# Optimization experiments

Hardware: AMD Instinct MI355X
Metric: run time of the kernel (lower is better)

Reference implementation:

```python
import jax, jax.numpy as jnp
import numpy as np
from jax import lax

B, H, V, L = 128, 256, 130, 100  # batch, hidden_size, vocab per stream, decode length


def _gru(x, h, wih, whh, bih, bhh):
    # torch.nn.GRUCell math
    gi = x @ wih.T + bih
    gh = h @ whh.T + bhh
    ir, iz, inn = jnp.split(gi, 3, axis=-1)
    hr, hz, hn = jnp.split(gh, 3, axis=-1)
    r = jax.nn.sigmoid(ir + hr)
    u = jax.nn.sigmoid(iz + hz)
    n = jnp.tanh(inn + r * hn)
    return (1.0 - u) * n + u * h


def _forward(z, gru1_wih, gru1_whh, gru1_bih, gru1_bhh,
             gru2_wih, gru2_whh, gru2_bih, gru2_bhh,
             ctx_wih, ctx_whh, ctx_bih, ctx_bhh,
             out_w, out_b, hid_w, hid_b, emb, length):
    b = z.shape[0]
    hidden = jnp.tanh(z @ hid_w.T + hid_b)                      # [B,H]
    h3 = jnp.broadcast_to(hidden[None], (3, b, hidden.shape[-1]))
    note0 = jnp.broadcast_to(emb[:, 0][:, None, :], (3, b, emb.shape[-1]))  # embed index 0
    vgru = jax.vmap(_gru)  # over the 3 parallel streams

    def step(carry, _):
        g1h, g2h, context, note = carry
        zb = jnp.broadcast_to(z[None], note.shape)
        g1h = vgru(jnp.concatenate([note, zb], -1), g1h,
                   gru1_wih, gru1_whh, gru1_bih, gru1_bhh)       # [3,B,H]
        unroll = g1h
        logits = []
        for i in range(3):  # fixed structural unroll (3 streams)
            ctx_in = jnp.concatenate([unroll[0], unroll[1], unroll[2]], -1)  # [B,3H]
            context = _gru(ctx_in, context, ctx_wih, ctx_whh, ctx_bih, ctx_bhh)
            h2 = _gru(jnp.concatenate([context, z], -1), g2h[i],
                      gru2_wih[i], gru2_whh[i], gru2_bih[i], gru2_bhh[i])
            g2h = g2h.at[i].set(h2)
            lg = (unroll[i] + h2) @ out_w[i].T + out_b[i]        # [B,V]
            logits.append(lg)
            ni = emb[i][jnp.argmax(lg, axis=-1)]                 # greedy sample -> embed
            note = note.at[i].set(ni)
            # NOTE: original code uses self.gru1[1] here (fixed index 1) -- kept faithful
            unroll = unroll.at[i].set(_gru(jnp.concatenate([ni, z], -1), unroll[i],
                                           gru1_wih[1], gru1_whh[1], gru1_bih[1], gru1_bhh[1]))
        return (g1h, g2h, context, note), jnp.stack(logits)     # [3,B,V]

    _, ys = lax.scan(step, (h3, h3, hidden, note0), None, length=length)
    return jnp.transpose(ys, (1, 2, 0, 3))                      # [3,B,L,V]


def setup_inputs() -> dict:
    key = jax.random.key(0)
    ks = jax.random.split(key, 18)
    s = 0.05
    n = lambda k, shp: jax.random.normal(k, shp, jnp.float32) * s
    return {
        "z": jax.random.normal(ks[0], (B, H), jnp.float32),
        "gru1_wih": n(ks[1], (3, 3 * H, 2 * H)),
        "gru1_whh": n(ks[2], (3, 3 * H, H)),
        "gru1_bih": n(ks[3], (3, 3 * H)),
        "gru1_bhh": n(ks[4], (3, 3 * H)),
        "gru2_wih": n(ks[5], (3, 3 * H, 2 * H)),
        "gru2_whh": n(ks[6], (3, 3 * H, H)),
        "gru2_bih": n(ks[7], (3, 3 * H)),
        "gru2_bhh": n(ks[8], (3, 3 * H)),
        "ctx_wih": n(ks[9], (3 * H, 3 * H)),
        "ctx_whh": n(ks[10], (3 * H, H)),
        "ctx_bih": n(ks[11], (3 * H,)),
        "ctx_bhh": n(ks[12], (3 * H,)),
        "out_w": n(ks[13], (3, V, H)),
        "out_b": n(ks[14], (3, V)),
        "hid_w": n(ks[15], (H, H)),
        "hid_b": n(ks[16], (H,)),
        "emb": n(ks[17], (3, V, H)),
        "length": L,
    }


def reference(z, gru1_wih, gru1_whh, gru1_bih, gru1_bhh,
              gru2_wih, gru2_whh, gru2_bih, gru2_bhh,
              ctx_wih, ctx_whh, ctx_bih, ctx_bhh,
              out_w, out_b, hid_w, hid_b, emb, length):
    return _forward(z, gru1_wih, gru1_whh, gru1_bih, gru1_bhh,
                    gru2_wih, gru2_whh, gru2_bih, gru2_bhh,
                    ctx_wih, ctx_whh, ctx_bih, ctx_bhh,
                    out_w, out_b, hid_w, hid_b, emb, length)
```

## Files before the change

### kernel.cpp

```cpp
#include <hip/hip_runtime.h>
#include <math.h>

#define B 128
#define H 256
#define V 130
#define L 100
#define G3 768

__device__ __forceinline__ float sigmoidf_(float x) { return 1.0f / (1.0f + expf(-x)); }

template <int NCHUNK>
__global__ __launch_bounds__(256) void gru_gates(
    const float* __restrict__ x0, const float* __restrict__ x1,
    const float* __restrict__ x2, const float* __restrict__ x3,
    const float* __restrict__ wih, int wih_k,
    const float* __restrict__ whh,
    const float* __restrict__ zadd, const float* __restrict__ bih,
    const float* __restrict__ bhh,
    float* __restrict__ out0, float* __restrict__ out1)
{
  __shared__ float xs[32][260];
  const int tid = threadIdx.x;
  const int r   = tid & 31;
  const int hc  = tid >> 5;
  const int row0 = blockIdx.y * 32;
  const int col  = blockIdx.x * 8 + hc;

  float giR = 0.f, giZ = 0.f, giN = 0.f;
  float ghR = 0.f, ghZ = 0.f, ghN = 0.f;
  float hold = 0.f;

  for (int c = 0; c < NCHUNK; ++c) {
    const float* src = (c == 0) ? x0 : (c == 1) ? x1 : (c == 2) ? x2 : x3;
    for (int j = tid; j < 32 * 64; j += 256) {
      const int rr = j >> 6, k4 = (j & 63) << 2;
      const float4 v = *reinterpret_cast<const float4*>(src + (size_t)(row0 + rr) * H + k4);
      *reinterpret_cast<float4*>(&xs[rr][k4]) = v;
    }
    __syncthreads();

    const bool is_h = (c == NCHUNK - 1);
    const float* wR;
    const float* wZ;
    const float* wN;
    if (is_h) {
      wR = whh + (size_t)(col) * 256;
      wZ = whh + (size_t)(256 + col) * 256;
      wN = whh + (size_t)(512 + col) * 256;
    } else {
      const float* wb = wih + c * 256;
      wR = wb + (size_t)(col) * wih_k;
      wZ = wb + (size_t)(256 + col) * wih_k;
      wN = wb + (size_t)(512 + col) * wih_k;
    }

    float aR = 0.f, aZ = 0.f, aN = 0.f;
#pragma unroll 8
    for (int k = 0; k < 256; k += 4) {
      const float4 xv = *reinterpret_cast<const float4*>(&xs[r][k]);
      const float4 vR = *reinterpret_cast<const float4*>(wR + k);
      const float4 vZ = *reinterpret_cast<const float4*>(wZ + k);
      const float4 vN = *reinterpret_cast<const float4*>(wN + k);
      aR += xv.x * vR.x; aR += xv.y * vR.y; aR += xv.z * vR.z; aR += xv.w * vR.w;
      aZ += xv.x * vZ.x; aZ += xv.y * vZ.y; aZ += xv.z * vZ.z; aZ += xv.w * vZ.w;
      aN += xv.x * vN.x; aN += xv.y * vN.y; aN += xv.z * vN.z; aN += xv.w * vN.w;
    }
    if (is_h) {
      ghR = aR; ghZ = aZ; ghN = aN;
      hold = xs[r][col];
    } else {
      giR += aR; giZ += aZ; giN += aN;
    }
    if (c != NCHUNK - 1) __syncthreads();
  }

  float bR, bZ, bN;
  if (zadd) {
    const float* zp = zadd + (size_t)(row0 + r) * G3;
    bR = zp[col]; bZ = zp[256 + col]; bN = zp[512 + col];
  } else {
    bR = bih[col]; bZ = bih[256 + col]; bN = bih[512 + col];
  }
  const float hR = ghR + bhh[col];
  const float hZ = ghZ + bhh[256 + col];
  const float hN = ghN + bhh[512 + col];

  const float rg = sigmoidf_(giR + bR + hR);
  const float ug = sigmoidf_(giZ + bZ + hZ);
  const float ng = tanhf(giN + bN + rg * hN);
  const float hnew = (1.f - ug) * ng + ug * hold;

  const size_t oidx = (size_t)(row0 + r) * H + col;
  out0[oidx] = hnew;
  if (out1) out1[oidx] = hnew;
}

__global__ __launch_bounds__(256) void out_argmax(
    const float* __restrict__ u, const float* __restrict__ h2,
    const float* __restrict__ ow, const float* __restrict__ ob,
    const float* __restrict__ embi,
    float* __restrict__ note_i, float* __restrict__ outp)
{
  __shared__ float s[8][260];
  const int tid = threadIdx.x;
  const int r = tid >> 5;
  const int l = tid & 31;
  const int row0 = blockIdx.x * 8;

  for (int j = tid; j < 8 * 64; j += 256) {
    const int rr = j >> 6, k4 = (j & 63) << 2;
    const float4 a = *reinterpret_cast<const float4*>(u  + (size_t)(row0 + rr) * H + k4);
    const float4 b = *reinterpret_cast<const float4*>(h2 + (size_t)(row0 + rr) * H + k4);
    float4 vv; vv.x = a.x + b.x; vv.y = a.y + b.y; vv.z = a.z + b.z; vv.w = a.w + b.w;
    *reinterpret_cast<float4*>(&s[rr][k4]) = vv;
  }
  __syncthreads();

  float best = -INFINITY;
  int bidx = 0;
  for (int m = 0; m < 5; ++m) {
    const int v = l + (m << 5);
    if (v < V) {
      float acc = 0.f;
      const float* wrow = ow + (size_t)v * H;
#pragma unroll 8
      for (int k = 0; k < 256; k += 4) {
        const float4 xv = *reinterpret_cast<const float4*>(&s[r][k]);
        const float4 wv = *reinterpret_cast<const float4*>(wrow + k);
        acc += xv.x * wv.x; acc += xv.y * wv.y; acc += xv.z * wv.z; acc += xv.w * wv.w;
      }
      acc += ob[v];
      outp[(size_t)(row0 + r) * (L * V) + v] = acc;
      if (acc > best) { best = acc; bidx = v; }
    }
  }
  for (int off = 16; off > 0; off >>= 1) {
    const float ov = __shfl_xor(best, off, 32);
    const int   oi = __shfl_xor(bidx, off, 32);
    if (ov > best || (ov == best && oi < bidx)) { best = ov; bidx = oi; }
  }
  const float* erow = embi + (size_t)bidx * H;
  float* nrow = note_i + (size_t)(row0 + r) * H;
  const int k0 = l * 8;
  *reinterpret_cast<float4*>(nrow + k0)     = *reinterpret_cast<const float4*>(erow + k0);
  *reinterpret_cast<float4*>(nrow + k0 + 4) = *reinterpret_cast<const float4*>(erow + k0 + 4);
}

__global__ __launch_bounds__(256) void hid_kernel(
    const float* __restrict__ z, const float* __restrict__ hw,
    const float* __restrict__ hb, float* __restrict__ hidden)
{
  __shared__ float xs[32][260];
  const int tid = threadIdx.x;
  const int r = tid & 31, hc = tid >> 5;
  const int row0 = blockIdx.y * 32;
  const int col = blockIdx.x * 8 + hc;
  for (int j = tid; j < 32 * 64; j += 256) {
    const int rr = j >> 6, k4 = (j & 63) << 2;
    *reinterpret_cast<float4*>(&xs[rr][k4]) =
        *reinterpret_cast<const float4*>(z + (size_t)(row0 + rr) * H + k4);
  }
  __syncthreads();
  float acc = 0.f;
  const float* wrow = hw + (size_t)col * H;
#pragma unroll 8
  for (int k = 0; k < 256; k += 4) {
    const float4 xv = *reinterpret_cast<const float4*>(&xs[r][k]);
    const float4 wv = *reinterpret_cast<const float4*>(wrow + k);
    acc += xv.x * wv.x; acc += xv.y * wv.y; acc += xv.z * wv.z; acc += xv.w * wv.w;
  }
  hidden[(size_t)(row0 + r) * H + col] = tanhf(acc + hb[col]);
}

__global__ __launch_bounds__(256) void zpre_kernel(
    const float* __restrict__ z, const float* __restrict__ wih,
    const float* __restrict__ bih, float* __restrict__ zout)
{
  __shared__ float xs[32][260];
  const int tid = threadIdx.x;
  const int r = tid & 31, hc = tid >> 5;
  const int row0 = blockIdx.y * 32;
  const int gr = blockIdx.x * 8 + hc;
  const int s = gr / 768;
  const int g = gr - s * 768;
  for (int j = tid; j < 32 * 64; j += 256) {
    const int rr = j >> 6, k4 = (j & 63) << 2;
    *reinterpret_cast<float4*>(&xs[rr][k4]) =
        *reinterpret_cast<const float4*>(z + (size_t)(row0 + rr) * H + k4);
  }
  __syncthreads();
  float acc = 0.f;
  const float* wrow = wih + (size_t)gr * 512 + 256;
#pragma unroll 8
  for (int k = 0; k < 256; k += 4) {
    const float4 xv = *reinterpret_cast<const float4*>(&xs[r][k]);
    const float4 wv = *reinterpret_cast<const float4*>(wrow + k);
    acc += xv.x * wv.x; acc += xv.y * wv.y; acc += xv.z * wv.z; acc += xv.w * wv.w;
  }
  zout[((size_t)(s * B + row0 + r)) * G3 + g] = acc + bih[gr];
}

__global__ __launch_bounds__(256) void init_copy(
    const float* __restrict__ hidden, float* __restrict__ g1h0,
    float* __restrict__ h20, float* __restrict__ ctx0)
{
  const int e = blockIdx.x * 256 + threadIdx.x;
  const float v = hidden[e];
  ctx0[e] = v;
  for (int s = 0; s < 3; ++s) {
    g1h0[(size_t)s * B * H + e] = v;
    h20[(size_t)s * B * H + e] = v;
  }
}

__global__ __launch_bounds__(256) void init_note(
    const float* __restrict__ emb, float* __restrict__ note)
{
  const int e = blockIdx.x * 256 + threadIdx.x;
  const int s = e / (B * H);
  const int c = e & (H - 1);
  note[e] = emb[(size_t)s * V * H + c];
}

extern "C" void kernel_launch(void* const* d_in, const int* in_sizes, int n_in,
                              void* d_out, int out_size, void* d_ws, size_t ws_size,
                              hipStream_t stream) {
  const float* z     = (const float*)d_in[0];
  const float* g1wih = (const float*)d_in[1];
  const float* g1whh = (const float*)d_in[2];
  const float* g1bih = (const float*)d_in[3];
  const float* g1bhh = (const float*)d_in[4];
  const float* g2wih = (const float*)d_in[5];
  const float* g2whh = (const float*)d_in[6];
  const float* g2bih = (const float*)d_in[7];
  const float* g2bhh = (const float*)d_in[8];
  const float* cwih  = (const float*)d_in[9];
  const float* cwhh  = (const float*)d_in[10];
  const float* cbih  = (const float*)d_in[11];
  const float* cbhh  = (const float*)d_in[12];
  const float* outw  = (const float*)d_in[13];
  const float* outb  = (const float*)d_in[14];
  const float* hidw  = (const float*)d_in[15];
  const float* hidb  = (const float*)d_in[16];
  const float* emb   = (const float*)d_in[17];
  float* out = (float*)d_out;

  float* ws = (float*)d_ws;
  size_t off = 0;
  auto alloc = [&](size_t n) { float* p = ws + off; off += n; return p; };
  float* hidden = alloc((size_t)B * H);
  float* Z1     = alloc((size_t)3 * B * G3);
  float* Z2     = alloc((size_t)3 * B * G3);
  float* g1h[2] = {alloc((size_t)3 * B * H), alloc((size_t)3 * B * H)};
  float* h2b[2] = {alloc((size_t)3 * B * H), alloc((size_t)3 * B * H)};
  float* ctx[2] = {alloc((size_t)B * H), alloc((size_t)B * H)};
  float* U0     = alloc((size_t)3 * B * H);
  float* U1     = alloc((size_t)3 * B * H);
  float* note   = alloc((size_t)3 * B * H);

  const dim3 blk(256);
  const dim3 grd32(32, 4);

  hid_kernel<<<grd32, blk, 0, stream>>>(z, hidw, hidb, hidden);
  zpre_kernel<<<dim3(288, 4), blk, 0, stream>>>(z, g1wih, g1bih, Z1);
  zpre_kernel<<<dim3(288, 4), blk, 0, stream>>>(z, g2wih, g2bih, Z2);
  init_copy<<<128, blk, 0, stream>>>(hidden, g1h[0], h2b[0], ctx[0]);
  init_note<<<384, blk, 0, stream>>>(emb, note);

  for (int t = 0; t < L; ++t) {
    const int rb = t & 1, wb = (t + 1) & 1;
    for (int s = 0; s < 3; ++s) {
      gru_gates<2><<<grd32, blk, 0, stream>>>(
          note + (size_t)s * B * H, g1h[rb] + (size_t)s * B * H, nullptr, nullptr,
          g1wih + (size_t)s * G3 * 512, 512, g1whh + (size_t)s * G3 * H,
          Z1 + (size_t)s * B * G3, nullptr, g1bhh + (size_t)s * G3,
          g1h[wb] + (size_t)s * B * H, U0 + (size_t)s * B * H);
    }
    for (int i = 0; i < 3; ++i) {
      const int j = 3 * t + i;
      const float* us[3];
      for (int s2 = 0; s2 < 3; ++s2)
        us[s2] = (s2 < i ? U1 : U0) + (size_t)s2 * B * H;
      gru_gates<4><<<grd32, blk, 0, stream>>>(
          us[0], us[1], us[2], ctx[j & 1],
          cwih, 768, cwhh,
          nullptr, cbih, cbhh,
          ctx[(j + 1) & 1], nullptr);
      gru_gates<2><<<grd32, blk, 0, stream>>>(
          ctx[(j + 1) & 1], h2b[rb] + (size_t)i * B * H, nullptr, nullptr,
          g2wih + (size_t)i * G3 * 512, 512, g2whh + (size_t)i * G3 * H,
          Z2 + (size_t)i * B * G3, nullptr, g2bhh + (size_t)i * G3,
          h2b[wb] + (size_t)i * B * H, nullptr);
      out_argmax<<<16, blk, 0, stream>>>(
          U0 + (size_t)i * B * H, h2b[wb] + (size_t)i * B * H,
          outw + (size_t)i * V * H, outb + (size_t)i * V, emb + (size_t)i * V * H,
          note + (size_t)i * B * H, out + (size_t)i * B * L * V + (size_t)t * V);
      gru_gates<2><<<grd32, blk, 0, stream>>>(
          note + (size_t)i * B * H, U0 + (size_t)i * B * H, nullptr, nullptr,
          g1wih + (size_t)1 * G3 * 512, 512, g1whh + (size_t)1 * G3 * H,
          Z1 + (size_t)1 * B * G3, nullptr, g1bhh + (size_t)1 * G3,
          U1 + (size_t)i * B * H, nullptr);
    }
  }
}
```

Measured before the change: 37.40 ms.

## Replace per-step kernel launches with a persistent kernel using grid barriers

Replaces roughly 1800 small kernel launches (5 per sub-step × 3 × 100 steps, plus the gru1 launches) with one persistent kernel of 256 workgroups that moves through the phases and synchronizes with a flag-based grid barrier in global memory. It also splits the K dimension of each GRU dot product across 4 lanes with shuffle reductions, and gives the output/argmax phase one row per workgroup. This removes launch overhead and gives better parallelism per phase, but adds spin-wait barrier cost. It relies on all 256 workgroups being co-resident, which holds on this device.

```diff
diff --git a/kernel.cpp b/kernel.cpp
--- a/kernel.cpp
+++ b/kernel.cpp
@@ -6,144 +6,268 @@
 #define V 130
 #define L 100
 #define G3 768
+#define BH (B*H)
+#define NWG 256
+#define NT 512
+
+#define OFF_FLAGS 0
+#define OFF_HID   256
+#define OFF_Z1    (OFF_HID + BH)
+#define OFF_Z2    (OFF_Z1 + 3*B*G3)
+#define OFF_G1HA  (OFF_Z2 + 3*B*G3)
+#define OFF_G1HB  (OFF_G1HA + 3*BH)
+#define OFF_H2A   (OFF_G1HB + 3*BH)
+#define OFF_H2B   (OFF_H2A + 3*BH)
+#define OFF_CTXA  (OFF_H2B + 3*BH)
+#define OFF_CTXB  (OFF_CTXA + BH)
+#define OFF_U0    (OFF_CTXB + BH)
+#define OFF_U1    (OFF_U0 + 3*BH)
+#define OFF_NOTE  (OFF_U1 + 3*BH)
 
 __device__ __forceinline__ float sigmoidf_(float x) { return 1.0f / (1.0f + expf(-x)); }
 
+__device__ __forceinline__ void grid_barrier(int* flags, int epoch) {
+  __syncthreads();
+  __threadfence();
+  if (threadIdx.x == 0)
+    __hip_atomic_store(flags + blockIdx.x, epoch, __ATOMIC_RELAXED, __HIP_MEMORY_SCOPE_AGENT);
+  if (threadIdx.x < 64) {
+    const int base = (int)threadIdx.x * 4;
+    for (;;) {
+      int m0 = __hip_atomic_load(flags + base + 0, __ATOMIC_RELAXED, __HIP_MEMORY_SCOPE_AGENT);
+      int m1 = __hip_atomic_load(flags + base + 1, __ATOMIC_RELAXED, __HIP_MEMORY_SCOPE_AGENT);
+      int m2 = __hip_atomic_load(flags + base + 2, __ATOMIC_RELAXED, __HIP_MEMORY_SCOPE_AGENT);
+      int m3 = __hip_atomic_load(flags + base + 3, __ATOMIC_RELAXED, __HIP_MEMORY_SCOPE_AGENT);
+      bool ok = (m0 >= epoch) & (m1 >= epoch) & (m2 >= epoch) & (m3 >= epoch);
+      if (__all(ok)) break;
+      __builtin_amdgcn_s_sleep(2);
+    }
+  }
+  __builtin_amdgcn_fence(__ATOMIC_ACQUIRE, "agent");
+  __syncthreads();
+}
+
 template <int NCHUNK>
-__global__ __launch_bounds__(256) void gru_gates(
-    const float* __restrict__ x0, const float* __restrict__ x1,
-    const float* __restrict__ x2, const float* __restrict__ x3,
-    const float* __restrict__ wih, int wih_k,
+__device__ void gru_phase(
+    const float* __restrict__ xc0, const float* __restrict__ xc1,
+    const float* __restrict__ xc2, const float* __restrict__ xc3,
+    const float* __restrict__ wih, int wih_stride,
     const float* __restrict__ whh,
-    const float* __restrict__ zadd, const float* __restrict__ bih,
+    const float* __restrict__ zadd,
+    const float* __restrict__ bih,
     const float* __restrict__ bhh,
-    float* __restrict__ out0, float* __restrict__ out1)
-{
-  __shared__ float xs[32][260];
-  const int tid = threadIdx.x;
-  const int r   = tid & 31;
-  const int hc  = tid >> 5;
-  const int row0 = blockIdx.y * 32;
-  const int col  = blockIdx.x * 8 + hc;
-
-  float giR = 0.f, giZ = 0.f, giN = 0.f;
-  float ghR = 0.f, ghZ = 0.f, ghN = 0.f;
-  float hold = 0.f;
-
+    float* __restrict__ out0, float* __restrict__ out1,
+    float* smem, int row0, int col0, int tid)
+{
+  __syncthreads();
+  const float* xc[4] = {xc0, xc1, xc2, xc3};
+#pragma unroll
   for (int c = 0; c < NCHUNK; ++c) {
-    const float* src = (c == 0) ? x0 : (c == 1) ? x1 : (c == 2) ? x2 : x3;
-    for (int j = tid; j < 32 * 64; j += 256) {
-      const int rr = j >> 6, k4 = (j & 63) << 2;
-      const float4 v = *reinterpret_cast<const float4*>(src + (size_t)(row0 + rr) * H + k4);
-      *reinterpret_cast<float4*>(&xs[rr][k4]) = v;
-    }
-    __syncthreads();
-
-    const bool is_h = (c == NCHUNK - 1);
-    const float* wR;
-    const float* wZ;
-    const float* wN;
-    if (is_h) {
-      wR = whh + (size_t)(col) * 256;
-      wZ = whh + (size_t)(256 + col) * 256;
-      wN = whh + (size_t)(512 + col) * 256;
+    const float* src = xc[c];
+#pragma unroll
+    for (int q = 0; q < 2; ++q) {
+      int idx = q * NT + tid;
+      int rr = idx >> 6;
+      int k4 = (idx & 63) << 2;
+      float4 v = *reinterpret_cast<const float4*>(src + (size_t)(row0 + rr) * H + k4);
+      *reinterpret_cast<float4*>(smem + c * 4160 + rr * 260 + k4) = v;
+    }
+  }
+  __syncthreads();
+
+  const int kq = tid & 3;
+  const int row_l = (tid >> 2) & 15;
+  const int col_l = tid >> 6;
+  const int col = col0 + col_l;
+
+  const int kstart = kq * (NCHUNK * 64);
+  const int c = kstart >> 8;
+  const int koff = kstart & 255;
+  const bool is_ih = (c < NCHUNK - 1);
+
+  const float* wb;
+  int wstr;
+  if (is_ih) { wstr = wih_stride; wb = wih + (size_t)col * wstr + (c * 256 + koff); }
+  else       { wstr = 256;        wb = whh + (size_t)col * 256 + koff; }
+  const float* wR = wb;
+  const float* wZ = wb + (size_t)256 * wstr;
+  const float* wN = wb + (size_t)512 * wstr;
+  const float* xr = smem + c * 4160 + row_l * 260 + koff;
+
+  float aR = 0.f, aZ = 0.f, aN = 0.f;
+  const int klen = NCHUNK * 64;
+#pragma unroll 8
+  for (int k = 0; k < klen; k += 4) {
+    float4 xv = *reinterpret_cast<const float4*>(xr + k);
+    float4 vR = *reinterpret_cast<const float4*>(wR + k);
+    float4 vZ = *reinterpret_cast<const float4*>(wZ + k);
+    float4 vN = *reinterpret_cast<const float4*>(wN + k);
+    aR += xv.x * vR.x; aR += xv.y * vR.y; aR += xv.z * vR.z; aR += xv.w * vR.w;
+    aZ += xv.x * vZ.x; aZ += xv.y * vZ.y; aZ += xv.z * vZ.z; aZ += xv.w * vZ.w;
+    aN += xv.x * vN.x; aN += xv.y * vN.y; aN += xv.z * vN.z; aN += xv.w * vN.w;
+  }
+  float aNi = is_ih ? aN : 0.f;
+  float aNh = is_ih ? 0.f : aN;
+#pragma unroll
+  for (int m = 1; m <= 2; m <<= 1) {
+    aR  += __shfl_xor(aR, m);
+    aZ  += __shfl_xor(aZ, m);
+    aNi += __shfl_xor(aNi, m);
+    aNh += __shfl_xor(aNh, m);
+  }
+  if (kq == 0) {
+    float bR, bZ, bN;
+    if (zadd) {
+      const float* zp = zadd + (size_t)(row0 + row_l) * G3;
+      bR = zp[col]; bZ = zp[256 + col]; bN = zp[512 + col];
     } else {
-      const float* wb = wih + c * 256;
-      wR = wb + (size_t)(col) * wih_k;
-      wZ = wb + (size_t)(256 + col) * wih_k;
-      wN = wb + (size_t)(512 + col) * wih_k;
-    }
-
-    float aR = 0.f, aZ = 0.f, aN = 0.f;
-#pragma unroll 8
-    for (int k = 0; k < 256; k += 4) {
-      const float4 xv = *reinterpret_cast<const float4*>(&xs[r][k]);
-      const float4 vR = *reinterpret_cast<const float4*>(wR + k);
-      const float4 vZ = *reinterpret_cast<const float4*>(wZ + k);
-      const float4 vN = *reinterpret_cast<const float4*>(wN + k);
-      aR += xv.x * vR.x; aR += xv.y * vR.y; aR += xv.z * vR.z; aR += xv.w * vR.w;
-      aZ += xv.x * vZ.x; aZ += xv.y * vZ.y; aZ += xv.z * vZ.z; aZ += xv.w * vZ.w;
-      aN += xv.x * vN.x; aN += xv.y * vN.y; aN += xv.z * vN.z; aN += xv.w * vN.w;
-    }
-    if (is_h) {
-      ghR = aR; ghZ = aZ; ghN = aN;
-      hold = xs[r][col];
-    } else {
-      giR += aR; giZ += aZ; giN += aN;
-    }
-    if (c != NCHUNK - 1) __syncthreads();
-  }
-
-  float bR, bZ, bN;
-  if (zadd) {
-    const float* zp = zadd + (size_t)(row0 + r) * G3;
-    bR = zp[col]; bZ = zp[256 + col]; bN = zp[512 + col];
-  } else {
-    bR = bih[col]; bZ = bih[256 + col]; bN = bih[512 + col];
-  }
-  const float hR = ghR + bhh[col];
-  const float hZ = ghZ + bhh[256 + col];
-  const float hN = ghN + bhh[512 + col];
-
-  const float rg = sigmoidf_(giR + bR + hR);
-  const float ug = sigmoidf_(giZ + bZ + hZ);
-  const float ng = tanhf(giN + bN + rg * hN);
-  const float hnew = (1.f - ug) * ng + ug * hold;
-
-  const size_t oidx = (size_t)(row0 + r) * H + col;
-  out0[oidx] = hnew;
-  if (out1) out1[oidx] = hnew;
-}
-
-__global__ __launch_bounds__(256) void out_argmax(
-    const float* __restrict__ u, const float* __restrict__ h2,
+      bR = bih[col]; bZ = bih[256 + col]; bN = bih[512 + col];
+    }
+    const float hR = bhh[col], hZ = bhh[256 + col], hN = bhh[512 + col];
+    const float hold = smem[(NCHUNK - 1) * 4160 + row_l * 260 + col];
+    const float rg = sigmoidf_(aR + bR + hR);
+    const float ug = sigmoidf_(aZ + bZ + hZ);
+    const float ng = tanhf(aNi + bN + rg * (aNh + hN));
+    const float hnew = (1.f - ug) * ng + ug * hold;
+    const size_t o = (size_t)(row0 + row_l) * H + col;
+    out0[o] = hnew;
+    if (out1) out1[o] = hnew;
+  }
+}
+
+__device__ void out_phase(
+    const float* __restrict__ u0i, const float* __restrict__ h2i,
     const float* __restrict__ ow, const float* __restrict__ ob,
     const float* __restrict__ embi,
-    float* __restrict__ note_i, float* __restrict__ outp)
-{
-  __shared__ float s[8][260];
-  const int tid = threadIdx.x;
-  const int r = tid >> 5;
-  const int l = tid & 31;
-  const int row0 = blockIdx.x * 8;
-
-  for (int j = tid; j < 8 * 64; j += 256) {
-    const int rr = j >> 6, k4 = (j & 63) << 2;
-    const float4 a = *reinterpret_cast<const float4*>(u  + (size_t)(row0 + rr) * H + k4);
-    const float4 b = *reinterpret_cast<const float4*>(h2 + (size_t)(row0 + rr) * H + k4);
-    float4 vv; vv.x = a.x + b.x; vv.y = a.y + b.y; vv.z = a.z + b.z; vv.w = a.w + b.w;
-    *reinterpret_cast<float4*>(&s[rr][k4]) = vv;
-  }
-  __syncthreads();
-
-  float best = -INFINITY;
-  int bidx = 0;
-  for (int m = 0; m < 5; ++m) {
-    const int v = l + (m << 5);
-    if (v < V) {
+    float* __restrict__ note_i, float* __restrict__ outp,
+    float* smem, int* sidx, int w, int tid)
+{
+  if (w >= B) return;
+  const int row = w;
+  __syncthreads();
+  if (tid < 64) {
+    float4 a = *reinterpret_cast<const float4*>(u0i + (size_t)row * H + tid * 4);
+    float4 b = *reinterpret_cast<const float4*>(h2i + (size_t)row * H + tid * 4);
+    float4 s4; s4.x = a.x + b.x; s4.y = a.y + b.y; s4.z = a.z + b.z; s4.w = a.w + b.w;
+    *reinterpret_cast<float4*>(smem + tid * 4) = s4;
+  }
+  __syncthreads();
+
+  const int v = tid >> 2, kq = tid & 3;
+#pragma unroll
+  for (int p = 0; p < 2; ++p) {
+    const int vv = v + p * 128;
+    if (vv < V) {
+      const float* wrow = ow + (size_t)vv * H + kq * 64;
+      const float* xr = smem + kq * 64;
       float acc = 0.f;
-      const float* wrow = ow + (size_t)v * H;
-#pragma unroll 8
-      for (int k = 0; k < 256; k += 4) {
-        const float4 xv = *reinterpret_cast<const float4*>(&s[r][k]);
-        const float4 wv = *reinterpret_cast<const float4*>(wrow + k);
+#pragma unroll 4
+      for (int k = 0; k < 64; k += 4) {
+        float4 xv = *reinterpret_cast<const float4*>(xr + k);
+        float4 wv = *reinterpret_cast<const float4*>(wrow + k);
         acc += xv.x * wv.x; acc += xv.y * wv.y; acc += xv.z * wv.z; acc += xv.w * wv.w;
       }
-      acc += ob[v];
-      outp[(size_t)(row0 + r) * (L * V) + v] = acc;
-      if (acc > best) { best = acc; bidx = v; }
-    }
-  }
-  for (int off = 16; off > 0; off >>= 1) {
-    const float ov = __shfl_xor(best, off, 32);
-    const int   oi = __shfl_xor(bidx, off, 32);
-    if (ov > best || (ov == best && oi < bidx)) { best = ov; bidx = oi; }
-  }
-  const float* erow = embi + (size_t)bidx * H;
-  float* nrow = note_i + (size_t)(row0 + r) * H;
-  const int k0 = l * 8;
-  *reinterpret_cast<float4*>(nrow + k0)     = *reinterpret_cast<const float4*>(erow + k0);
-  *reinterpret_cast<float4*>(nrow + k0 + 4) = *reinterpret_cast<const float4*>(erow + k0 + 4);
+      acc += __shfl_xor(acc, 1);
+      acc += __shfl_xor(acc, 2);
+      if (kq == 0) {
+        acc += ob[vv];
+        outp[vv] = acc;
+        smem[260 * 4 + vv] = acc;
+      }
+    }
+  }
+  __syncthreads();
+  if (tid < 64) {
+    float* vals = smem + 260 * 4;
+    float bv = vals[tid]; int bi = tid;
+    float c1 = vals[64 + tid];
+    if (c1 > bv) { bv = c1; bi = 64 + tid; }
+    if (tid < 2) { float c2 = vals[128 + tid]; if (c2 > bv) { bv = c2; bi = 128 + tid; } }
+#pragma unroll
+    for (int off = 32; off; off >>= 1) {
+      float ov = __shfl_down(bv, off);
+      int oi = __shfl_down(bi, off);
+      if (ov > bv || (ov == bv && oi < bi)) { bv = ov; bi = oi; }
+    }
+    if (tid == 0) *sidx = bi;
+  }
+  __syncthreads();
+  const int idx = *sidx;
+  if (tid < 64) {
+    float4 e = *reinterpret_cast<const float4*>(embi + (size_t)idx * H + tid * 4);
+    *reinterpret_cast<float4*>(note_i + (size_t)row * H + tid * 4) = e;
+  }
+}
+
+__global__ __launch_bounds__(NT) void decoder_persistent(
+    const float* __restrict__ g1wih, const float* __restrict__ g1whh,
+    const float* __restrict__ g1bhh,
+    const float* __restrict__ g2wih, const float* __restrict__ g2whh,
+    const float* __restrict__ g2bhh,
+    const float* __restrict__ cwih, const float* __restrict__ cwhh,
+    const float* __restrict__ cbih, const float* __restrict__ cbhh,
+    const float* __restrict__ outw, const float* __restrict__ outb,
+    const float* __restrict__ emb,
+    float* __restrict__ out, float* __restrict__ wsf)
+{
+  __shared__ float smem[4 * 4160];
+  __shared__ int sidx;
+  int* flags = reinterpret_cast<int*>(wsf) + OFF_FLAGS;
+  float* Z1   = wsf + OFF_Z1;
+  float* Z2   = wsf + OFF_Z2;
+  float* g1h[2] = {wsf + OFF_G1HA, wsf + OFF_G1HB};
+  float* h2b[2] = {wsf + OFF_H2A,  wsf + OFF_H2B};
+  float* ctx[2] = {wsf + OFF_CTXA, wsf + OFF_CTXB};
+  float* U0   = wsf + OFF_U0;
+  float* U1   = wsf + OFF_U1;
+  float* note = wsf + OFF_NOTE;
+
+  const int w = blockIdx.x, tid = threadIdx.x;
+  const int rb = w & 7, cb = w >> 3;
+  const int row0 = rb * 16, col0 = cb * 8;
+  int ep = 0;
+
+  for (int t = 0; t < L; ++t) {
+    const int rbk = t & 1, wbk = (t + 1) & 1;
+    for (int s = 0; s < 3; ++s) {
+      gru_phase<2>(note + (size_t)s * BH, g1h[rbk] + (size_t)s * BH, nullptr, nullptr,
+                   g1wih + (size_t)s * G3 * 512, 512, g1whh + (size_t)s * G3 * H,
+                   Z1 + (size_t)s * B * G3, nullptr, g1bhh + (size_t)s * G3,
+                   g1h[wbk] + (size_t)s * BH, U0 + (size_t)s * BH,
+                   smem, row0, col0, tid);
+    }
+    grid_barrier(flags, ++ep);
+    for (int i = 0; i < 3; ++i) {
+      const int j = 3 * t + i;
+      const float* us0 = (0 < i ? U1 : U0) + 0 * BH;
+      const float* us1 = (1 < i ? U1 : U0) + 1 * BH;
+      const float* us2 = (2 < i ? U1 : U0) + 2 * BH;
+      gru_phase<4>(us0, us1, us2, ctx[j & 1],
+                   cwih, G3, cwhh,
+                   nullptr, cbih, cbhh,
+                   ctx[(j + 1) & 1], nullptr,
+                   smem, row0, col0, tid);
+      grid_barrier(flags, ++ep);
+      gru_phase<2>(ctx[(j + 1) & 1], h2b[rbk] + (size_t)i * BH, nullptr, nullptr,
+                   g2wih + (size_t)i * G3 * 512, 512, g2whh + (size_t)i * G3 * H,
+                   Z2 + (size_t)i * B * G3, nullptr, g2bhh + (size_t)i * G3,
+                   h2b[wbk] + (size_t)i * BH, nullptr,
+                   smem, row0, col0, tid);
+      grid_barrier(flags, ++ep);
+      out_phase(U0 + (size_t)i * BH, h2b[wbk] + (size_t)i * BH,
+                outw + (size_t)i * V * H, outb + (size_t)i * V, emb + (size_t)i * V * H,
+                note + (size_t)i * BH,
+                out + (size_t)i * B * L * V + (size_t)w * L * V + (size_t)t * V,
+                smem, &sidx, w, tid);
+      grid_barrier(flags, ++ep);
+      gru_phase<2>(note + (size_t)i * BH, U0 + (size_t)i * BH, nullptr, nullptr,
+                   g1wih + (size_t)1 * G3 * 512, 512, g1whh + (size_t)1 * G3 * H,
+                   Z1 + (size_t)1 * B * G3, nullptr, g1bhh + (size_t)1 * G3,
+                   U1 + (size_t)i * BH, nullptr,
+                   smem, row0, col0, tid);
+      grid_barrier(flags, ++ep);
+    }
+  }
 }
 
 __global__ __launch_bounds__(256) void hid_kernel(
@@ -155,8 +279,8 @@
   const int r = tid & 31, hc = tid >> 5;
   const int row0 = blockIdx.y * 32;
   const int col = blockIdx.x * 8 + hc;
-  for (int j = tid; j < 32 * 64; j += 256) {
-    const int rr = j >> 6, k4 = (j & 63) << 2;
+  for (int jj = tid; jj < 32 * 64; jj += 256) {
+    const int rr = jj >> 6, k4 = (jj & 63) << 2;
     *reinterpret_cast<float4*>(&xs[rr][k4]) =
         *reinterpret_cast<const float4*>(z + (size_t)(row0 + rr) * H + k4);
   }
@@ -181,10 +305,10 @@
   const int r = tid & 31, hc = tid >> 5;
   const int row0 = blockIdx.y * 32;
   const int gr = blockIdx.x * 8 + hc;
-  const int s = gr / 768;
-  const int g = gr - s * 768;
-  for (int j = tid; j < 32 * 64; j += 256) {
-    const int rr = j >> 6, k4 = (j & 63) << 2;
+  const int s = gr / G3;
+  const int g = gr - s * G3;
+  for (int jj = tid; jj < 32 * 64; jj += 256) {
+    const int rr = jj >> 6, k4 = (jj & 63) << 2;
     *reinterpret_cast<float4*>(&xs[rr][k4]) =
         *reinterpret_cast<const float4*>(z + (size_t)(row0 + rr) * H + k4);
   }
@@ -208,8 +332,8 @@
   const float v = hidden[e];
   ctx0[e] = v;
   for (int s = 0; s < 3; ++s) {
-    g1h0[(size_t)s * B * H + e] = v;
-    h20[(size_t)s * B * H + e] = v;
+    g1h0[(size_t)s * BH + e] = v;
+    h20[(size_t)s * BH + e] = v;
   }
 }
 
@@ -217,10 +341,12 @@
     const float* __restrict__ emb, float* __restrict__ note)
 {
   const int e = blockIdx.x * 256 + threadIdx.x;
-  const int s = e / (B * H);
+  const int s = e / BH;
   const int c = e & (H - 1);
   note[e] = emb[(size_t)s * V * H + c];
 }
+
+__global__ void zero_flags(int* flags) { flags[threadIdx.x] = 0; }
 
 extern "C" void kernel_launch(void* const* d_in, const int* in_sizes, int n_in,
                               void* d_out, int out_size, void* d_ws, size_t ws_size,
@@ -244,62 +370,19 @@
   const float* hidb  = (const float*)d_in[16];
   const float* emb   = (const float*)d_in[17];
   float* out = (float*)d_out;
-
-  float* ws = (float*)d_ws;
-  size_t off = 0;
-  auto alloc = [&](size_t n) { float* p = ws + off; off += n; return p; };
-  float* hidden = alloc((size_t)B * H);
-  float* Z1     = alloc((size_t)3 * B * G3);
-  float* Z2     = alloc((size_t)3 * B * G3);
-  float* g1h[2] = {alloc((size_t)3 * B * H), alloc((size_t)3 * B * H)};
-  float* h2b[2] = {alloc((size_t)3 * B * H), alloc((size_t)3 * B * H)};
-  float* ctx[2] = {alloc((size_t)B * H), alloc((size_t)B * H)};
-  float* U0     = alloc((size_t)3 * B * H);
-  float* U1     = alloc((size_t)3 * B * H);
-  float* note   = alloc((size_t)3 * B * H);
+  float* wsf = (float*)d_ws;
+  int* flags = (int*)d_ws;
 
   const dim3 blk(256);
-  const dim3 grd32(32, 4);
-
-  hid_kernel<<<grd32, blk, 0, stream>>>(z, hidw, hidb, hidden);
-  zpre_kernel<<<dim3(288, 4), blk, 0, stream>>>(z, g1wih, g1bih, Z1);
-  zpre_kernel<<<dim3(288, 4), blk, 0, stream>>>(z, g2wih, g2bih, Z2);
-  init_copy<<<128, blk, 0, stream>>>(hidden, g1h[0], h2b[0], ctx[0]);
-  init_note<<<384, blk, 0, stream>>>(emb, note);
-
-  for (int t = 0; t < L; ++t) {
-    const int rb = t & 1, wb = (t + 1) & 1;
-    for (int s = 0; s < 3; ++s) {
-      gru_gates<2><<<grd32, blk, 0, stream>>>(
-          note + (size_t)s * B * H, g1h[rb] + (size_t)s * B * H, nullptr, nullptr,
-          g1wih + (size_t)s * G3 * 512, 512, g1whh + (size_t)s * G3 * H,
-          Z1 + (size_t)s * B * G3, nullptr, g1bhh + (size_t)s * G3,
-          g1h[wb] + (size_t)s * B * H, U0 + (size_t)s * B * H);
-    }
-    for (int i = 0; i < 3; ++i) {
-      const int j = 3 * t + i;
-      const float* us[3];
-      for (int s2 = 0; s2 < 3; ++s2)
-        us[s2] = (s2 < i ? U1 : U0) + (size_t)s2 * B * H;
-      gru_gates<4><<<grd32, blk, 0, stream>>>(
-          us[0], us[1], us[2], ctx[j & 1],
-          cwih, 768, cwhh,
-          nullptr, cbih, cbhh,
-          ctx[(j + 1) & 1], nullptr);
-      gru_gates<2><<<grd32, blk, 0, stream>>>(
-          ctx[(j + 1) & 1], h2b[rb] + (size_t)i * B * H, nullptr, nullptr,
-          g2wih + (size_t)i * G3 * 512, 512, g2whh + (size_t)i * G3 * H,
-          Z2 + (size_t)i * B * G3, nullptr, g2bhh + (size_t)i * G3,
-          h2b[wb] + (size_t)i * B * H, nullptr);
-      out_argmax<<<16, blk, 0, stream>>>(
-          U0 + (size_t)i * B * H, h2b[wb] + (size_t)i * B * H,
-          outw + (size_t)i * V * H, outb + (size_t)i * V, emb + (size_t)i * V * H,
-          note + (size_t)i * B * H, out + (size_t)i * B * L * V + (size_t)t * V);
-      gru_gates<2><<<grd32, blk, 0, stream>>>(
-          note + (size_t)i * B * H, U0 + (size_t)i * B * H, nullptr, nullptr,
-          g1wih + (size_t)1 * G3 * 512, 512, g1whh + (size_t)1 * G3 * H,
-          Z1 + (size_t)1 * B * G3, nullptr, g1bhh + (size_t)1 * G3,
-          U1 + (size_t)i * B * H, nullptr);
-    }
-  }
-}
+  hid_kernel<<<dim3(32, 4), blk, 0, stream>>>(z, hidw, hidb, wsf + OFF_HID);
+  zpre_kernel<<<dim3(288, 4), blk, 0, stream>>>(z, g1wih, g1bih, wsf + OFF_Z1);
+  zpre_kernel<<<dim3(288, 4), blk, 0, stream>>>(z, g2wih, g2bih, wsf + OFF_Z2);
+  init_copy<<<128, blk, 0, stream>>>(wsf + OFF_HID, wsf + OFF_G1HA,
+                                     wsf + OFF_H2A, wsf + OFF_CTXA);
+  init_note<<<384, blk, 0, stream>>>(emb, wsf + OFF_NOTE);
+  zero_flags<<<1, 256, 0, stream>>>(flags);
+
+  decoder_persistent<<<NWG, NT, 0, stream>>>(
+      g1wih, g1whh, g1bhh, g2wih, g2whh, g2bhh,
+      cwih, cwhh, cbih, cbhh, outw, outb, emb, out, wsf);
+}
```

Result: slower. 102.3 ms (+173.5%).
